# Performance work log

Measured on AMD Instinct MI355X. Metric: run time of the kernel, lower is better.

Reference implementation:

```python
import jax, jax.numpy as jnp
import numpy as np

NUM_EMBEDDINGS = 512
EMBEDDING_DIM = 64
COMMITMENT_COST = 0.25


def setup_inputs() -> dict:
    key = jax.random.key(0)
    k1, k2 = jax.random.split(key)
    inputs = jax.random.normal(k1, (32, EMBEDDING_DIM, 64, 64), dtype=jnp.float32)  # NCHW
    # nn.Embedding weight init: uniform(-1/K, 1/K)
    embedding = jax.random.uniform(
        k2, (NUM_EMBEDDINGS, EMBEDDING_DIM), dtype=jnp.float32,
        minval=-1.0 / NUM_EMBEDDINGS, maxval=1.0 / NUM_EMBEDDINGS)
    return {"inputs": inputs, "embedding": embedding}


def reference(inputs, embedding):
    # NCHW -> NHWC, flatten to [N, D]
    x = jnp.transpose(inputs, (0, 2, 3, 1))
    flat = x.reshape(-1, EMBEDDING_DIM)  # [N, D]
    distances = (jnp.sum(flat * flat, axis=1, keepdims=True)
                 + jnp.sum(embedding * embedding, axis=1)
                 - 2.0 * flat @ embedding.T)
    idx = jnp.argmin(distances, axis=1)  # [N]
    # gather codebook rows (equivalent to one-hot @ embedding, fused)
    quantized = jnp.take(embedding, idx, axis=0).reshape(x.shape)
    e_latent_loss = jnp.mean((jax.lax.stop_gradient(quantized) - x) ** 2)
    q_latent_loss = jnp.mean((quantized - jax.lax.stop_gradient(x)) ** 2)
    loss = q_latent_loss + COMMITMENT_COST * e_latent_loss
    # straight-through estimator
    quantized = x + jax.lax.stop_gradient(quantized - x)
    out = jnp.transpose(quantized, (0, 3, 1, 2))  # back to NCHW
    return out, loss
```

## Files before the change

### kernel.cpp

```cpp
#include <hip/hip_runtime.h>


#define D 64
#define K_EMB 512
#define HW 4096
#define CHW (D * HW)
#define OUT_ELEMS 8388608
#define NB_MAIN 1024
#define SWZ(r) ((((r) ^ ((r) >> 2))) & 7)

typedef __attribute__((ext_vector_type(8))) short short8;
typedef __attribute__((ext_vector_type(4))) float f32x4;

__device__ __forceinline__ unsigned short f2bf(float f) {
    unsigned u = __float_as_uint(f);
    u += 0x7FFFu + ((u >> 16) & 1u);
    return (unsigned short)(u >> 16);
}
__device__ __forceinline__ float bf2f(unsigned short h) {
    return __uint_as_float(((unsigned)h) << 16);
}
__device__ __forceinline__ unsigned umin32(unsigned a, unsigned b) { return a <= b ? a : b; }
__device__ __forceinline__ unsigned cvtpk(float lo, float hi) {
    unsigned r;
    asm("v_cvt_pk_bf16_f32 %0, %1, %2" : "=v"(r) : "v"(lo), "v"(hi));
    return r;
}

__global__ void vq_prep(const float* __restrict__ emb, unsigned short* __restrict__ ebf,
                        float* __restrict__ npm) {
    int k = blockIdx.x * 256 + threadIdx.x;
    const float4* e4 = reinterpret_cast<const float4*>(emb + k * D);
    unsigned short h[D];
    float acc = 0.f;
#pragma unroll
    for (int i = 0; i < 16; ++i) {
        float4 v = e4[i];
        acc += v.x * v.x + v.y * v.y + v.z * v.z + v.w * v.w;
        h[4 * i + 0] = f2bf(v.x); h[4 * i + 1] = f2bf(v.y);
        h[4 * i + 2] = f2bf(v.z); h[4 * i + 3] = f2bf(v.w);
    }
    npm[k] = -0.5f * (1.0f + acc);
    uint4* dst = reinterpret_cast<uint4*>(ebf + k * D);
#pragma unroll
    for (int i = 0; i < 8; ++i) {
        uint4 p;
        p.x = (unsigned)h[8 * i + 0] | ((unsigned)h[8 * i + 1] << 16);
        p.y = (unsigned)h[8 * i + 2] | ((unsigned)h[8 * i + 3] << 16);
        p.z = (unsigned)h[8 * i + 4] | ((unsigned)h[8 * i + 5] << 16);
        p.w = (unsigned)h[8 * i + 6] | ((unsigned)h[8 * i + 7] << 16);
        dst[i] = p;
    }
}

__global__ __launch_bounds__(256, 4) void vq_mfma(const float* __restrict__ in,
                                                  const unsigned short* __restrict__ ebf,
                                                  const float* __restrict__ npm,
                                                  const float* __restrict__ emb,
                                                  float* __restrict__ out,
                                                  float* __restrict__ partials) {
    __shared__ __align__(16) char ldsX[16384];
    __shared__ __align__(16) unsigned keysS[4][128];
    __shared__ float red4[4];

    const int tid = threadIdx.x;
    const int lane = tid & 63;
    const int w = tid >> 6;
    const int col = lane & 15;
    const int dg = lane >> 4;
    const int bid = ((blockIdx.x & 7) << 7) | (blockIdx.x >> 3);
    const int n = bid >> 5;
    const int hw0 = (bid & 31) << 7;

    {
        const int rw = (tid & 31) * 4;
        const int cg = tid >> 5;
        const float* xb = in + n * CHW + cg * 8 * HW + hw0 + rw;
        f32x4 v[8];
#pragma unroll
        for (int ch = 0; ch < 8; ++ch)
            v[ch] = *reinterpret_cast<const f32x4*>(xb + ch * HW);
#pragma unroll
        for (int j = 0; j < 4; ++j) {
            const int r = rw + j;
            uint4 p;
            p.x = cvtpk(v[0][j], v[1][j]);
            p.y = cvtpk(v[2][j], v[3][j]);
            p.z = cvtpk(v[4][j], v[5][j]);
            p.w = cvtpk(v[6][j], v[7][j]);
            *reinterpret_cast<uint4*>(ldsX + r * 128 + ((cg ^ SWZ(r)) * 16)) = p;
        }
    }

    unsigned best[8][4];
#pragma unroll
    for (int rt = 0; rt < 8; ++rt)
#pragma unroll
        for (int i = 0; i < 4; ++i) best[rt][i] = 0xFFFFFFFFu;

    const short8* e8 = reinterpret_cast<const short8*>(ebf);
#pragma unroll 1
    for (int g = 0; g < 2; ++g) {
        const int kb = w * 128 + g * 64 + col;
        short8 ef[4][2];
        float npv[4];
#pragma unroll
        for (int ct = 0; ct < 4; ++ct) {
            const int k = kb + ct * 16;
            ef[ct][0] = e8[k * 8 + dg];
            ef[ct][1] = e8[k * 8 + 4 + dg];
            npv[ct] = npm[k];
        }
        if (g == 0) __syncthreads();

#pragma unroll
        for (int rt = 0; rt < 8; ++rt) {
            const int row = rt * 16 + col;
            short8 a0 = *reinterpret_cast<const short8*>(
                ldsX + row * 128 + ((dg ^ SWZ(row)) * 16));
            short8 a1 = *reinterpret_cast<const short8*>(
                ldsX + row * 128 + (((4 + dg) ^ SWZ(row)) * 16));
#pragma unroll
            for (int ct = 0; ct < 4; ++ct) {
                f32x4 acc = {npv[ct], npv[ct], npv[ct], npv[ct]};
                acc = __builtin_amdgcn_mfma_f32_16x16x32_bf16(a0, ef[ct][0], acc, 0, 0, 0);
                acc = __builtin_amdgcn_mfma_f32_16x16x32_bf16(a1, ef[ct][1], acc, 0, 0, 0);
                const unsigned kc = (unsigned)(kb + ct * 16);
#pragma unroll
                for (int i = 0; i < 4; ++i) {
                    unsigned key = (__float_as_uint(acc[i]) & 0xFFFFFE00u) | kc;
                    best[rt][i] = umin32(best[rt][i], key);
                }
            }
        }
    }

#pragma unroll
    for (int rt = 0; rt < 8; ++rt)
#pragma unroll
        for (int i = 0; i < 4; ++i) {
            unsigned k = best[rt][i];
#pragma unroll
            for (int s = 1; s < 16; s <<= 1)
                k = umin32(k, (unsigned)__shfl_xor((int)k, s, 64));
            if (col == 0) keysS[w][rt * 16 + dg * 4 + i] = k;
        }
    __syncthreads();

    const int rg = tid & 31;
    const int cs = tid >> 5;
    uint4 q0 = *reinterpret_cast<const uint4*>(&keysS[0][rg * 4]);
    uint4 q1 = *reinterpret_cast<const uint4*>(&keysS[1][rg * 4]);
    uint4 q2 = *reinterpret_cast<const uint4*>(&keysS[2][rg * 4]);
    uint4 q3 = *reinterpret_cast<const uint4*>(&keysS[3][rg * 4]);
    int kk[4];
    kk[0] = (int)(umin32(umin32(q0.x, q1.x), umin32(q2.x, q3.x)) & 511u);
    kk[1] = (int)(umin32(umin32(q0.y, q1.y), umin32(q2.y, q3.y)) & 511u);
    kk[2] = (int)(umin32(umin32(q0.z, q1.z), umin32(q2.z, q3.z)) & 511u);
    kk[3] = (int)(umin32(umin32(q0.w, q1.w), umin32(q2.w, q3.w)) & 511u);
    float ej[4][8];
#pragma unroll
    for (int j = 0; j < 4; ++j) {
        const f32x4* ep = reinterpret_cast<const f32x4*>(emb + kk[j] * D + cs * 8);
        *reinterpret_cast<f32x4*>(&ej[j][0]) = ep[0];
        *reinterpret_cast<f32x4*>(&ej[j][4]) = ep[1];
    }
    float lsum = 0.f;
#pragma unroll
    for (int j = 0; j < 4; ++j) {
        const int r = rg * 4 + j;
        short8 x8 = *reinterpret_cast<const short8*>(
            ldsX + r * 128 + ((cs ^ SWZ(r)) * 16));
#pragma unroll
        for (int t = 0; t < 8; ++t) {
            float d = ej[j][t] - bf2f((unsigned short)x8[t]);
            lsum = fmaf(d, d, lsum);
        }
    }
    float* obase = out + n * CHW + hw0 + rg * 4;
#pragma unroll
    for (int t = 0; t < 8; ++t) {
        f32x4 st = {ej[0][t], ej[1][t], ej[2][t], ej[3][t]};
        __builtin_nontemporal_store(st, reinterpret_cast<f32x4*>(obase + (cs * 8 + t) * HW));
    }

#pragma unroll
    for (int s = 1; s < 64; s <<= 1) lsum += __shfl_xor(lsum, s, 64);
    if (lane == 0) red4[w] = lsum;
    __syncthreads();
    if (tid == 0) partials[bid] = red4[0] + red4[1] + red4[2] + red4[3];
}

__global__ void vq_finalize(const float* __restrict__ partials, float* __restrict__ loss) {
    __shared__ float s[256];
    float a = 0.f;
    for (int i = threadIdx.x; i < NB_MAIN; i += 256) a += partials[i];
    s[threadIdx.x] = a;
    __syncthreads();
    for (int t = 128; t > 0; t >>= 1) {
        if ((int)threadIdx.x < t) s[threadIdx.x] += s[threadIdx.x + t];
        __syncthreads();
    }
    if (threadIdx.x == 0) loss[0] = 1.25f * s[0] * (1.0f / (float)OUT_ELEMS);
}

extern "C" void kernel_launch(void* const* d_in, const int* in_sizes, int n_in,
                              void* d_out, int out_size, void* d_ws, size_t ws_size,
                              hipStream_t stream) {
    const float* in = (const float*)d_in[0];
    const float* emb = (const float*)d_in[1];
    float* out = (float*)d_out;
    unsigned short* ebf = (unsigned short*)d_ws;
    float* npm = (float*)((char*)d_ws + 65536);
    float* partials = (float*)((char*)d_ws + 67584);

    vq_prep<<<2, 256, 0, stream>>>(emb, ebf, npm);
    vq_mfma<<<NB_MAIN, 256, 0, stream>>>(in, ebf, npm, emb, out, partials);
    vq_finalize<<<1, 256, 0, stream>>>(partials, out + OUT_ELEMS);
}
```

Measured before the change: 33.06 us.

## Give each wave its own rows over all codes and derive loss algebraically

Each wave now owns 32 rows and scans all 512 codes, instead of each wave scanning a 128-code slice for all 128 rows. This removes the block-level __syncthreads and the cross-wave key merge, and the A fragments stay in registers across the whole code loop. The loss is rebuilt from the ||x||^2 sum and the minimum distance key (npm is -0.5(1+||e||^2)), with a constant correction applied in finalize. That replaces the gather-and-subtract pass but relies on the truncated bf16-accumulated keys, which could hurt loss precision.

```diff
diff --git a/kernel.cpp b/kernel.cpp
--- a/kernel.cpp
+++ b/kernel.cpp
@@ -7,6 +7,7 @@
 #define CHW (D * HW)
 #define OUT_ELEMS 8388608
 #define NB_MAIN 1024
+#define NPART 4096
 #define SWZ(r) ((((r) ^ ((r) >> 2))) & 7)
 
 typedef __attribute__((ext_vector_type(8))) short short8;
@@ -16,9 +17,6 @@
     unsigned u = __float_as_uint(f);
     u += 0x7FFFu + ((u >> 16) & 1u);
     return (unsigned short)(u >> 16);
-}
-__device__ __forceinline__ float bf2f(unsigned short h) {
-    return __uint_as_float(((unsigned)h) << 16);
 }
 __device__ __forceinline__ unsigned umin32(unsigned a, unsigned b) { return a <= b ? a : b; }
 __device__ __forceinline__ unsigned cvtpk(float lo, float hi) {
@@ -59,9 +57,8 @@
                                                   const float* __restrict__ emb,
                                                   float* __restrict__ out,
                                                   float* __restrict__ partials) {
-    __shared__ __align__(16) char ldsX[16384];
-    __shared__ __align__(16) unsigned keysS[4][128];
-    __shared__ float red4[4];
+    __shared__ __align__(16) char ldsX[4][4096];
+    __shared__ __align__(16) unsigned keysW[4][32];
 
     const int tid = threadIdx.x;
     const int lane = tid & 63;
@@ -72,36 +69,53 @@
     const int n = bid >> 5;
     const int hw0 = (bid & 31) << 7;
 
+    const int r4 = lane & 7;
+    const int cs = lane >> 3;
+    const int rbase = w * 32 + r4 * 4;
+    char* X = ldsX[w];
+    float xs = 0.f;
     {
-        const int rw = (tid & 31) * 4;
-        const int cg = tid >> 5;
-        const float* xb = in + n * CHW + cg * 8 * HW + hw0 + rw;
+        const float* xb = in + n * CHW + cs * 8 * HW + hw0 + rbase;
         f32x4 v[8];
 #pragma unroll
         for (int ch = 0; ch < 8; ++ch)
             v[ch] = *reinterpret_cast<const f32x4*>(xb + ch * HW);
 #pragma unroll
+        for (int ch = 0; ch < 8; ++ch)
+#pragma unroll
+            for (int j = 0; j < 4; ++j) xs = fmaf(v[ch][j], v[ch][j], xs);
+#pragma unroll
         for (int j = 0; j < 4; ++j) {
-            const int r = rw + j;
+            const int rl = r4 * 4 + j;
             uint4 p;
             p.x = cvtpk(v[0][j], v[1][j]);
             p.y = cvtpk(v[2][j], v[3][j]);
             p.z = cvtpk(v[4][j], v[5][j]);
             p.w = cvtpk(v[6][j], v[7][j]);
-            *reinterpret_cast<uint4*>(ldsX + r * 128 + ((cg ^ SWZ(r)) * 16)) = p;
-        }
-    }
-
-    unsigned best[8][4];
-#pragma unroll
-    for (int rt = 0; rt < 8; ++rt)
+            *reinterpret_cast<uint4*>(X + rl * 128 + ((cs ^ SWZ(rl)) * 16)) = p;
+        }
+    }
+
+    short8 af[2][2];
+#pragma unroll
+    for (int rt = 0; rt < 2; ++rt) {
+        const int rl = rt * 16 + col;
+#pragma unroll
+        for (int kh = 0; kh < 2; ++kh)
+            af[rt][kh] = *reinterpret_cast<const short8*>(
+                X + rl * 128 + (((kh * 4 + dg) ^ SWZ(rl)) * 16));
+    }
+
+    unsigned best[2][4];
+#pragma unroll
+    for (int rt = 0; rt < 2; ++rt)
 #pragma unroll
         for (int i = 0; i < 4; ++i) best[rt][i] = 0xFFFFFFFFu;
 
     const short8* e8 = reinterpret_cast<const short8*>(ebf);
 #pragma unroll 1
-    for (int g = 0; g < 2; ++g) {
-        const int kb = w * 128 + g * 64 + col;
+    for (int g = 0; g < 8; ++g) {
+        const int kb = g * 64 + col;
         short8 ef[4][2];
         float npv[4];
 #pragma unroll
@@ -111,20 +125,13 @@
             ef[ct][1] = e8[k * 8 + 4 + dg];
             npv[ct] = npm[k];
         }
-        if (g == 0) __syncthreads();
-
-#pragma unroll
-        for (int rt = 0; rt < 8; ++rt) {
-            const int row = rt * 16 + col;
-            short8 a0 = *reinterpret_cast<const short8*>(
-                ldsX + row * 128 + ((dg ^ SWZ(row)) * 16));
-            short8 a1 = *reinterpret_cast<const short8*>(
-                ldsX + row * 128 + (((4 + dg) ^ SWZ(row)) * 16));
+#pragma unroll
+        for (int rt = 0; rt < 2; ++rt) {
 #pragma unroll
             for (int ct = 0; ct < 4; ++ct) {
                 f32x4 acc = {npv[ct], npv[ct], npv[ct], npv[ct]};
-                acc = __builtin_amdgcn_mfma_f32_16x16x32_bf16(a0, ef[ct][0], acc, 0, 0, 0);
-                acc = __builtin_amdgcn_mfma_f32_16x16x32_bf16(a1, ef[ct][1], acc, 0, 0, 0);
+                acc = __builtin_amdgcn_mfma_f32_16x16x32_bf16(af[rt][0], ef[ct][0], acc, 0, 0, 0);
+                acc = __builtin_amdgcn_mfma_f32_16x16x32_bf16(af[rt][1], ef[ct][1], acc, 0, 0, 0);
                 const unsigned kc = (unsigned)(kb + ct * 16);
 #pragma unroll
                 for (int i = 0; i < 4; ++i) {
@@ -135,29 +142,25 @@
         }
     }
 
-#pragma unroll
-    for (int rt = 0; rt < 8; ++rt)
+    float csum = 0.f;
+#pragma unroll
+    for (int rt = 0; rt < 2; ++rt)
 #pragma unroll
         for (int i = 0; i < 4; ++i) {
             unsigned k = best[rt][i];
 #pragma unroll
             for (int s = 1; s < 16; s <<= 1)
                 k = umin32(k, (unsigned)__shfl_xor((int)k, s, 64));
-            if (col == 0) keysS[w][rt * 16 + dg * 4 + i] = k;
-        }
-    __syncthreads();
-
-    const int rg = tid & 31;
-    const int cs = tid >> 5;
-    uint4 q0 = *reinterpret_cast<const uint4*>(&keysS[0][rg * 4]);
-    uint4 q1 = *reinterpret_cast<const uint4*>(&keysS[1][rg * 4]);
-    uint4 q2 = *reinterpret_cast<const uint4*>(&keysS[2][rg * 4]);
-    uint4 q3 = *reinterpret_cast<const uint4*>(&keysS[3][rg * 4]);
+            if (col == 0) {
+                keysW[w][rt * 16 + dg * 4 + i] = k;
+                csum += __uint_as_float(k & 0xFFFFFE00u);
+            }
+        }
+
     int kk[4];
-    kk[0] = (int)(umin32(umin32(q0.x, q1.x), umin32(q2.x, q3.x)) & 511u);
-    kk[1] = (int)(umin32(umin32(q0.y, q1.y), umin32(q2.y, q3.y)) & 511u);
-    kk[2] = (int)(umin32(umin32(q0.z, q1.z), umin32(q2.z, q3.z)) & 511u);
-    kk[3] = (int)(umin32(umin32(q0.w, q1.w), umin32(q2.w, q3.w)) & 511u);
+#pragma unroll
+    for (int j = 0; j < 4; ++j) kk[j] = (int)(keysW[w][r4 * 4 + j] & 511u);
+
     float ej[4][8];
 #pragma unroll
     for (int j = 0; j < 4; ++j) {
@@ -165,43 +168,31 @@
         *reinterpret_cast<f32x4*>(&ej[j][0]) = ep[0];
         *reinterpret_cast<f32x4*>(&ej[j][4]) = ep[1];
     }
-    float lsum = 0.f;
-#pragma unroll
-    for (int j = 0; j < 4; ++j) {
-        const int r = rg * 4 + j;
-        short8 x8 = *reinterpret_cast<const short8*>(
-            ldsX + r * 128 + ((cs ^ SWZ(r)) * 16));
-#pragma unroll
-        for (int t = 0; t < 8; ++t) {
-            float d = ej[j][t] - bf2f((unsigned short)x8[t]);
-            lsum = fmaf(d, d, lsum);
-        }
-    }
-    float* obase = out + n * CHW + hw0 + rg * 4;
+    float* obase = out + n * CHW + hw0 + rbase;
 #pragma unroll
     for (int t = 0; t < 8; ++t) {
         f32x4 st = {ej[0][t], ej[1][t], ej[2][t], ej[3][t]};
         __builtin_nontemporal_store(st, reinterpret_cast<f32x4*>(obase + (cs * 8 + t) * HW));
     }
 
-#pragma unroll
-    for (int s = 1; s < 64; s <<= 1) lsum += __shfl_xor(lsum, s, 64);
-    if (lane == 0) red4[w] = lsum;
-    __syncthreads();
-    if (tid == 0) partials[bid] = red4[0] + red4[1] + red4[2] + red4[3];
+    float q = xs - 2.0f * csum;
+#pragma unroll
+    for (int s = 1; s < 64; s <<= 1) q += __shfl_xor(q, s, 64);
+    if (lane == 0) partials[bid * 4 + w] = q;
 }
 
 __global__ void vq_finalize(const float* __restrict__ partials, float* __restrict__ loss) {
     __shared__ float s[256];
     float a = 0.f;
-    for (int i = threadIdx.x; i < NB_MAIN; i += 256) a += partials[i];
+    for (int i = threadIdx.x; i < NPART; i += 256) a += partials[i];
     s[threadIdx.x] = a;
     __syncthreads();
     for (int t = 128; t > 0; t >>= 1) {
         if ((int)threadIdx.x < t) s[threadIdx.x] += s[threadIdx.x + t];
         __syncthreads();
     }
-    if (threadIdx.x == 0) loss[0] = 1.25f * s[0] * (1.0f / (float)OUT_ELEMS);
+    if (threadIdx.x == 0)
+        loss[0] = 1.25f * (s[0] - 131072.0f) * (1.0f / (float)OUT_ELEMS);
 }
 
 extern "C" void kernel_launch(void* const* d_in, const int* in_sizes, int n_in,
```

After: 53.75 us. +62.6%, slower.
